# Kernel optimization log

Measured on AMD Instinct MI355X. Metric: run time of the kernel, lower is better.

The kernel has to match this reference:

```python
import jax, jax.numpy as jnp
import numpy as np

D_MODEL = 1024
N_HEADS = 16
HEAD_DIM = D_MODEL // N_HEADS
D_FF = 4096
ROPE_RANK = 16
LN_EPS = 1e-5


def _ln(x, g, b):
    mu = jnp.mean(x, axis=-1, keepdims=True)
    var = jnp.mean((x - mu) ** 2, axis=-1, keepdims=True)
    return (x - mu) * jax.lax.rsqrt(var + LN_EPS) * g + b


def _rope(x, A, B_):
    # x: [B, T, D]; learned low-rank additive correction to sin/cos tables
    B, T, D = x.shape
    pos = jnp.arange(T, dtype=jnp.float32)
    theta = 1.0 / (10000.0 ** (jnp.arange(0, D, 2, dtype=jnp.float32) / D))  # [D/2]
    angles = pos[:, None] * theta[None, :]                                   # [T, D/2]
    sin_pos, cos_pos = jnp.sin(angles), jnp.cos(angles)
    base = jnp.concatenate([sin_pos, cos_pos], axis=-1)                      # [T, D]
    learned = (base @ A) @ B_                                                # [T, D]
    l_sin, l_cos = jnp.split(learned, 2, axis=-1)
    sin_f = sin_pos + l_sin                                                  # [T, D/2]
    cos_f = cos_pos + l_cos
    xe, xo = x[..., ::2], x[..., 1::2]
    re = xe * cos_f[None] - xo * sin_f[None]
    ro = xe * sin_f[None] + xo * cos_f[None]
    return jnp.stack([re, ro], axis=-1).reshape(B, T, D)


def setup_inputs() -> dict:
    key = jax.random.key(0)
    ks = jax.random.split(key, 20)
    B, T = 2, 2048
    s = 1.0 / np.sqrt(D_MODEL)
    sf = 1.0 / np.sqrt(D_FF)
    sr = 1.0 / np.sqrt(ROPE_RANK)
    return {
        "tgt": jax.random.normal(ks[0], (B, T, D_MODEL), jnp.float32),
        "Wq": jax.random.normal(ks[1], (D_MODEL, D_MODEL), jnp.float32) * s,
        "bq": jnp.zeros((D_MODEL,), jnp.float32),
        "Wk": jax.random.normal(ks[2], (D_MODEL, D_MODEL), jnp.float32) * s,
        "bk": jnp.zeros((D_MODEL,), jnp.float32),
        "Wv": jax.random.normal(ks[3], (D_MODEL, D_MODEL), jnp.float32) * s,
        "bv": jnp.zeros((D_MODEL,), jnp.float32),
        "Wo": jax.random.normal(ks[4], (D_MODEL, D_MODEL), jnp.float32) * s,
        "bo": jnp.zeros((D_MODEL,), jnp.float32),
        "W1": jax.random.normal(ks[5], (D_MODEL, D_FF), jnp.float32) * s,
        "b1": jnp.zeros((D_FF,), jnp.float32),
        "W2": jax.random.normal(ks[6], (D_FF, D_MODEL), jnp.float32) * sf,
        "b2": jnp.zeros((D_MODEL,), jnp.float32),
        "ln1_g": jnp.ones((D_MODEL,), jnp.float32),
        "ln1_b": jnp.zeros((D_MODEL,), jnp.float32),
        "ln2_g": jnp.ones((D_MODEL,), jnp.float32),
        "ln2_b": jnp.zeros((D_MODEL,), jnp.float32),
        "rope_A": jax.random.normal(ks[7], (D_MODEL, ROPE_RANK), jnp.float32) * s,
        "rope_B": jax.random.normal(ks[8], (ROPE_RANK, D_MODEL), jnp.float32) * sr,
    }


def reference(tgt, Wq, bq, Wk, bk, Wv, bv, Wo, bo, W1, b1, W2, b2,
              ln1_g, ln1_b, ln2_g, ln2_b, rope_A, rope_B):
    x = tgt
    B, T, D = x.shape
    q = _rope(x @ Wq + bq, rope_A, rope_B)
    k = _rope(x @ Wk + bk, rope_A, rope_B)
    v = x @ Wv + bv
    # [B, H, T, hd]
    q = q.reshape(B, T, N_HEADS, HEAD_DIM).transpose(0, 2, 1, 3)
    k = k.reshape(B, T, N_HEADS, HEAD_DIM).transpose(0, 2, 1, 3)
    v = v.reshape(B, T, N_HEADS, HEAD_DIM).transpose(0, 2, 1, 3)
    scores = jnp.einsum("bhqd,bhkd->bhqk", q, k) / np.sqrt(HEAD_DIM)
    attn = jax.nn.softmax(scores, axis=-1)  # no mask: module applies none
    ctx = jnp.einsum("bhqk,bhkd->bhqd", attn, v)
    ctx = ctx.transpose(0, 2, 1, 3).reshape(B, T, D)
    x = x + (ctx @ Wo + bo)
    x = _ln(x, ln1_g, ln1_b)
    ff = jax.nn.relu(x @ W1 + b1) @ W2 + b2
    x = _ln(x + ff, ln2_g, ln2_b)
    return x
```

## Files before the change

### kernel.cpp

```cpp
#include <hip/hip_runtime.h>
#include <math.h>

typedef unsigned short u16;
typedef unsigned int u32;
typedef __attribute__((ext_vector_type(8))) short short8v;
typedef __attribute__((ext_vector_type(4))) float f32x4;

__device__ __forceinline__ u16 f2bf(float f) {
    u32 u = __float_as_uint(f);
    u32 r = (u + 0x7fffu + ((u >> 16) & 1u)) >> 16;
    return (u16)r;
}

#define GLOAD_LDS(g, l)                                                        \
    __builtin_amdgcn_global_load_lds(                                          \
        (const __attribute__((address_space(1))) void*)(g),                    \
        (__attribute__((address_space(3))) void*)(l), 16, 0, 0)

#define SCHED_FENCE() __builtin_amdgcn_sched_barrier(0)

#define ROPE_LOG2C (13.287712379549449f / 512.0f)

__device__ __forceinline__ void cast_body(const float* __restrict__ x,
                                          u16* __restrict__ y, int L, int tid) {
    const int gid = L * 256 + tid;
    float4 v = ((const float4*)x)[gid];
    ushort4 o;
    o.x = f2bf(v.x); o.y = f2bf(v.y); o.z = f2bf(v.z); o.w = f2bf(v.w);
    ((ushort4*)y)[gid] = o;
}

__device__ __forceinline__ void tcast64_body(const float* __restrict__ S,
                                             u16* __restrict__ Dt, int K, int N,
                                             int n0, int k0, int tid,
                                             char* smem) {
    float (*tile)[65] = (float (*)[65])smem;
    const int tx = tid & 15, ty = tid >> 4;
#pragma unroll
    for (int i = 0; i < 4; i++) {
        const int kr = ty + 16 * i;
        const float4 v = *(const float4*)&S[(size_t)(k0 + kr) * N + n0 + tx * 4];
        tile[kr][tx * 4 + 0] = v.x;
        tile[kr][tx * 4 + 1] = v.y;
        tile[kr][tx * 4 + 2] = v.z;
        tile[kr][tx * 4 + 3] = v.w;
    }
    __syncthreads();
#pragma unroll
    for (int i = 0; i < 4; i++) {
        const int nr = ty + 16 * i;
        ushort4 o;
        o.x = f2bf(tile[tx * 4 + 0][nr]);
        o.y = f2bf(tile[tx * 4 + 1][nr]);
        o.z = f2bf(tile[tx * 4 + 2][nr]);
        o.w = f2bf(tile[tx * 4 + 3][nr]);
        *(ushort4*)&Dt[(size_t)(n0 + nr) * K + k0 + tx * 4] = o;
    }
}

__device__ __forceinline__ void rope1_body(const float* __restrict__ A,
                                           float* __restrict__ P, int blk,
                                           int tid, char* smem) {
    float (*sc)[17]  = (float (*)[17])(smem);
    float (*cc)[17]  = (float (*)[17])(smem + 1088);
    float (*Als)[17] = (float (*)[17])(smem + 2176);
    float (*Alc)[17] = (float (*)[17])(smem + 3264);
    const int tt = tid >> 4, rr = tid & 15;
    const int t = blk * 16 + tt;
    float acc = 0.f;
    for (int i0 = 0; i0 < 512; i0 += 16) {
        __syncthreads();
        {
            const int i = i0 + rr;
            const float th = exp2f(-(float)i * ROPE_LOG2C);
            const float ang = (float)t * th;
            sc[tt][rr] = sinf(ang);
            cc[tt][rr] = cosf(ang);
            Als[tt][rr] = A[(i0 + tt) * 16 + rr];
            Alc[tt][rr] = A[(512 + i0 + tt) * 16 + rr];
        }
        __syncthreads();
#pragma unroll
        for (int ii = 0; ii < 16; ++ii)
            acc = fmaf(sc[tt][ii], Als[ii][rr],
                       fmaf(cc[tt][ii], Alc[ii][rr], acc));
    }
    P[t * 16 + rr] = acc;
}

__global__ __launch_bounds__(256) void prep_k(
    const float* __restrict__ tgt, u16* __restrict__ tgtb,
    const float* __restrict__ Wq, u16* __restrict__ Wqt,
    const float* __restrict__ Wk, u16* __restrict__ Wkt,
    const float* __restrict__ Wv, u16* __restrict__ Wvt,
    const float* __restrict__ Wo, u16* __restrict__ Wot,
    const float* __restrict__ W1, u16* __restrict__ W1t,
    const float* __restrict__ W2, u16* __restrict__ W2t,
    const float* __restrict__ rA, float* __restrict__ Pp) {
    __shared__ char smem[64 * 65 * 4];
    const int L = blockIdx.x, tid = threadIdx.x;
    if (L < 128) {
        rope1_body(rA, Pp, L, tid, smem);
    } else if (L < 4224) {
        cast_body(tgt, tgtb, L - 128, tid);
    } else if (L < 5248) {
        const int i = L - 4224;
        const int r = i >> 8, j = i & 255;
        const float* S = r == 0 ? Wq : (r == 1 ? Wk : (r == 2 ? Wv : Wo));
        u16* Dt = r == 0 ? Wqt : (r == 1 ? Wkt : (r == 2 ? Wvt : Wot));
        tcast64_body(S, Dt, 1024, 1024, (j & 15) * 64, (j >> 4) * 64, tid, smem);
    } else if (L < 6272) {
        const int j = L - 5248;
        tcast64_body(W1, W1t, 1024, 4096, (j & 63) * 64, (j >> 6) * 64, tid, smem);
    } else {
        const int j = L - 6272;
        tcast64_body(W2, W2t, 4096, 1024, (j & 15) * 64, (j >> 4) * 64, tid, smem);
    }
}

__global__ __launch_bounds__(256) void vtrans_k(const u16* __restrict__ vv,
                                                u16* __restrict__ Vt) {
    __shared__ u16 tile[32][33];
    const int key0 = blockIdx.x * 32, d0 = blockIdx.y * 32, bh = blockIdx.z;
    const int b = bh >> 4, h = bh & 15;
    const int tx = threadIdx.x & 31, ty = threadIdx.x >> 5;
#pragma unroll
    for (int i = 0; i < 4; i++)
        tile[ty + 8 * i][tx] =
            vv[(size_t)(b * 2048 + key0 + ty + 8 * i) * 1024 + h * 64 + d0 + tx];
    __syncthreads();
#pragma unroll
    for (int i = 0; i < 4; i++) {
        const int d = d0 + ty + 8 * i;
        const int key = key0 + tx;
        const int ksw = (key & ~63) | ((((key >> 3) & 7) ^ (d & 7)) << 3) | (key & 7);
        Vt[((size_t)bh * 64 + d) * 2048 + ksw] = tile[tx][ty + 8 * i];
    }
}

__global__ void rope2_k(const float* __restrict__ P, const float* __restrict__ Bw,
                        float* __restrict__ sf, float* __restrict__ cf) {
    const int gid = blockIdx.x * blockDim.x + threadIdx.x;
    if (gid >= 2048 * 512) return;
    const int t = gid >> 9, i = gid & 511;
    float ls = 0.f, lc = 0.f;
#pragma unroll
    for (int r = 0; r < 16; ++r) {
        const float p = P[t * 16 + r];
        ls = fmaf(p, Bw[r * 1024 + i], ls);
        lc = fmaf(p, Bw[r * 1024 + 512 + i], lc);
    }
    const float th = exp2f(-(float)i * ROPE_LOG2C);
    const float ang = (float)t * th;
    sf[gid] = sinf(ang) + ls;
    cf[gid] = cosf(ang) + lc;
}

__device__ __forceinline__ void xcd_tile(int L, int xn, int rn, int rm,
                                         int& tm, int& tn) {
    const int xcd = L & 7, i = L >> 3;
    const int cx = xcd % xn, cy = xcd / xn;
    tn = cx * rn + (i % rn);
    tm = cy * rm + (i / rn);
}

enum { EP_NONE = 0, EP_RELU = 3, EP_PART = 4 };

template <int EPI, bool CBF, int BN>
__global__ __launch_bounds__(256) void mgemm_k(
    const u16* __restrict__ A, const u16* __restrict__ Bt,
    const float* __restrict__ bias, void* __restrict__ Cp,
    void* __restrict__ Cp2, int M, int N, int K, int lda, int ldb,
    int xn, int rn, int rm, int mtiles) {
    constexpr int NT = BN / 32;
    __shared__ u16 As[3 * 128 * 32];
    __shared__ u16 Bs[3 * BN * 32];
    const int tid = threadIdx.x;
    const int w = tid >> 6, l = tid & 63;
    const int quad = l >> 4, lr = l & 15;
    const int wr = w >> 1, wc = w & 1;
    int tm, tn;
    xcd_tile(blockIdx.x, xn, rn, rm, tm, tn);
    int kh = 0;
    if (tm >= mtiles) { kh = 1; tm -= mtiles; }
    const u16* Ak = A + (size_t)kh * K;
    const u16* Bk = Bt + (size_t)kh * K;
    void* Co = kh ? Cp2 : Cp;
    const int m0 = tm * 128, n0 = tn * BN;

    const int srow = w * 16 + (l >> 2);
    const int scol = (((l & 3) ^ ((l >> 3) & 3)) * 8);
    const u16* ag0 = Ak + (size_t)(m0 + srow) * lda + scol;
    const u16* ag1 = Ak + (size_t)(m0 + 64 + srow) * lda + scol;
    const u16* bg0 = Bk + (size_t)(n0 + srow) * ldb + scol;
    const u16* bg1 = Bk + (size_t)(n0 + 64 + srow) * ldb + scol;

    f32x4 acc[4][NT];
#pragma unroll
    for (int i = 0; i < 4; i++)
#pragma unroll
        for (int j = 0; j < NT; j++) acc[i][j] = (f32x4)(0.0f);

    {
        GLOAD_LDS(ag0, As + w * 512);
        GLOAD_LDS(ag1, As + 2048 + w * 512);
        GLOAD_LDS(bg0, Bs + w * 512);
        if (BN == 128) GLOAD_LDS(bg1, Bs + 2048 + w * 512);
        GLOAD_LDS(ag0 + 32, As + 4096 + w * 512);
        GLOAD_LDS(ag1 + 32, As + 4096 + 2048 + w * 512);
        GLOAD_LDS(bg0 + 32, Bs + BN * 32 + w * 512);
        if (BN == 128) GLOAD_LDS(bg1 + 32, Bs + BN * 32 + 2048 + w * 512);
    }

    const int niter = K >> 5;
    const int xsw = ((lr >> 1) & 3) << 3;
    int bc = 0, bs = 2;
    for (int i = 0; i < niter; ++i) {
        SCHED_FENCE();
        if (i + 1 < niter) {
            if (BN == 128) asm volatile("s_waitcnt vmcnt(4) lgkmcnt(0)" ::: "memory");
            else           asm volatile("s_waitcnt vmcnt(3) lgkmcnt(0)" ::: "memory");
        } else {
            asm volatile("s_waitcnt vmcnt(0) lgkmcnt(0)" ::: "memory");
        }
        __builtin_amdgcn_s_barrier();
        SCHED_FENCE();
        if (i + 2 < niter) {
            const int kk = (i + 2) << 5;
            u16* Ab = As + bs * 4096;
            u16* Bb = Bs + bs * (BN * 32);
            GLOAD_LDS(ag0 + kk, Ab + w * 512);
            GLOAD_LDS(ag1 + kk, Ab + 2048 + w * 512);
            GLOAD_LDS(bg0 + kk, Bb + w * 512);
            if (BN == 128) GLOAD_LDS(bg1 + kk, Bb + 2048 + w * 512);
        }
        const u16* Ac = As + bc * 4096;
        const u16* Bc = Bs + bc * (BN * 32);
        short8v af[4], bf[NT];
#pragma unroll
        for (int mt = 0; mt < 4; ++mt)
            af[mt] = *(const short8v*)&Ac[(wr * 64 + mt * 16 + lr) * 32 +
                                          ((quad << 3) ^ xsw)];
#pragma unroll
        for (int nt = 0; nt < NT; ++nt)
            bf[nt] = *(const short8v*)&Bc[(wc * (BN / 2) + nt * 16 + lr) * 32 +
                                          ((quad << 3) ^ xsw)];
#pragma unroll
        for (int mt = 0; mt < 4; ++mt)
#pragma unroll
            for (int nt = 0; nt < NT; ++nt)
                acc[mt][nt] = __builtin_amdgcn_mfma_f32_16x16x32_bf16(
                    af[mt], bf[nt], acc[mt][nt], 0, 0, 0);
        bc = (bc == 2) ? 0 : bc + 1;
        bs = (bs == 2) ? 0 : bs + 1;
    }

#pragma unroll
    for (int mt = 0; mt < 4; ++mt) {
#pragma unroll
        for (int nt = 0; nt < NT; ++nt) {
            const int n = n0 + wc * (BN / 2) + nt * 16 + lr;
            const float bb = (EPI == EP_PART) ? 0.0f : bias[n];
#pragma unroll
            for (int reg = 0; reg < 4; ++reg) {
                const int m = m0 + wr * 64 + mt * 16 + quad * 4 + reg;
                float v = acc[mt][nt][reg] + bb;
                if (EPI == EP_RELU) v = fmaxf(v, 0.f);
                if (CBF) ((u16*)Co)[(size_t)m * N + n] = f2bf(v);
                else     ((float*)Co)[(size_t)m * N + n] = v;
            }
        }
    }
}

__global__ __launch_bounds__(256) void mqkv_k(
    const u16* __restrict__ A, const u16* __restrict__ Bt,
    const float* __restrict__ bq, const float* __restrict__ bk,
    const float* __restrict__ bv, const float* __restrict__ sf,
    const float* __restrict__ cf, u16* __restrict__ out) {
    const int K = 1024;
    __shared__ u16 As[3 * 128 * 32];
    __shared__ u16 Bs[3 * 128 * 32];
    const int tid = threadIdx.x;
    const int w = tid >> 6, l = tid & 63;
    const int quad = l >> 4, lr = l & 15;
    const int wr = w >> 1, wc = w & 1;
    int tm, tn;
    xcd_tile(blockIdx.x, 4, 6, 16, tm, tn);
    const int m0 = tm * 128, n0 = tn * 128;

    const int srow = w * 16 + (l >> 2);
    const int scol = (((l & 3) ^ ((l >> 3) & 3)) * 8);
    const u16* ag0 = A + (size_t)(m0 + srow) * K + scol;
    const u16* ag1 = A + (size_t)(m0 + 64 + srow) * K + scol;
    const u16* bg0 = Bt + (size_t)(n0 + srow) * K + scol;
    const u16* bg1 = Bt + (size_t)(n0 + 64 + srow) * K + scol;

    f32x4 acc[4][4];
#pragma unroll
    for (int i = 0; i < 4; i++)
#pragma unroll
        for (int j = 0; j < 4; j++) acc[i][j] = (f32x4)(0.0f);

    {
        GLOAD_LDS(ag0, As + w * 512);
        GLOAD_LDS(ag1, As + 2048 + w * 512);
        GLOAD_LDS(bg0, Bs + w * 512);
        GLOAD_LDS(bg1, Bs + 2048 + w * 512);
        GLOAD_LDS(ag0 + 32, As + 4096 + w * 512);
        GLOAD_LDS(ag1 + 32, As + 4096 + 2048 + w * 512);
        GLOAD_LDS(bg0 + 32, Bs + 4096 + w * 512);
        GLOAD_LDS(bg1 + 32, Bs + 4096 + 2048 + w * 512);
    }
    const int xsw = ((lr >> 1) & 3) << 3;
    int bc = 0, bsb = 2;
    for (int i = 0; i < 32; ++i) {
        SCHED_FENCE();
        if (i + 1 < 32) {
            asm volatile("s_waitcnt vmcnt(4) lgkmcnt(0)" ::: "memory");
        } else {
            asm volatile("s_waitcnt vmcnt(0) lgkmcnt(0)" ::: "memory");
        }
        __builtin_amdgcn_s_barrier();
        SCHED_FENCE();
        if (i + 2 < 32) {
            const int kk = (i + 2) << 5;
            u16* Ab = As + bsb * 4096;
            u16* Bb = Bs + bsb * 4096;
            GLOAD_LDS(ag0 + kk, Ab + w * 512);
            GLOAD_LDS(ag1 + kk, Ab + 2048 + w * 512);
            GLOAD_LDS(bg0 + kk, Bb + w * 512);
            GLOAD_LDS(bg1 + kk, Bb + 2048 + w * 512);
        }
        const u16* Ac = As + bc * 4096;
        const u16* Bc = Bs + bc * 4096;
        short8v af[4], bf[4];
#pragma unroll
        for (int mt = 0; mt < 4; ++mt)
            af[mt] = *(const short8v*)&Ac[(wr * 64 + mt * 16 + lr) * 32 +
                                          ((quad << 3) ^ xsw)];
#pragma unroll
        for (int nt = 0; nt < 4; ++nt)
            bf[nt] = *(const short8v*)&Bc[(wc * 64 + nt * 16 + lr) * 32 +
                                          ((quad << 3) ^ xsw)];
#pragma unroll
        for (int mt = 0; mt < 4; ++mt)
#pragma unroll
            for (int nt = 0; nt < 4; ++nt)
                acc[mt][nt] = __builtin_amdgcn_mfma_f32_16x16x32_bf16(
                    af[mt], bf[nt], acc[mt][nt], 0, 0, 0);
        bc = (bc == 2) ? 0 : bc + 1;
        bsb = (bsb == 2) ? 0 : bsb + 1;
    }

    const int which = n0 >> 10;
    const float* bias = which == 0 ? bq : (which == 1 ? bk : bv);
    const bool doRope = which < 2;
    u16* Cp = out + (size_t)which * 4096 * 1024;

#pragma unroll
    for (int mt = 0; mt < 4; ++mt) {
#pragma unroll
        for (int nt = 0; nt < 4; ++nt) {
            const int n = n0 + wc * 64 + nt * 16 + lr;
            const int col = n & 1023;
            const float bb = bias[col];
#pragma unroll
            for (int reg = 0; reg < 4; ++reg) {
                const int m = m0 + wr * 64 + mt * 16 + quad * 4 + reg;
                float v = acc[mt][nt][reg] + bb;
                const float partner = __shfl_xor(v, 1);
                int colw = col;
                if (doRope) {
                    const int t = m & 2047;
                    const int fi = col >> 1;
                    const float svv = sf[t * 512 + fi];
                    const float cvv = cf[t * 512 + fi];
                    v = (col & 1) ? fmaf(partner, svv, v * cvv)
                                  : fmaf(v, cvv, -partner * svv);
                    if (which == 0) v *= 0.125f;
                    colw = (col & ~63) | ((((col >> 3) & 7) ^ (m & 7)) << 3) |
                           (col & 7);
                }
                Cp[(size_t)m * 1024 + colw] = f2bf(v);
            }
        }
    }
}

__global__ __launch_bounds__(256, 3) void mattn_k(
    const u16* __restrict__ Q, const u16* __restrict__ Kg,
    const u16* __restrict__ Vt, u16* __restrict__ O) {
    __shared__ u16 QPs[128 * 64];
    __shared__ u16 Ks[2][64 * 64];
    __shared__ u16 Vs[2][64 * 64];
    const int tid = threadIdx.x;
    const int w = tid >> 6, l = tid & 63;
    const int quad = l >> 4, lr = l & 15;
    const int L = blockIdx.x;
    const int bh = (L & 7) * 4 + ((L >> 3) & 3);
    const int b = bh >> 4, h = bh & 15;
    const int row0 = (L >> 5) * 128;
    const size_t base = (size_t)b * 2048 * 1024 + (size_t)h * 64;
    const size_t vbase = (size_t)bh * 64 * 2048;

    const int dr = l >> 3;
    const int dc = (l & 7) * 8;
    const int g0 = w * 2, g1 = g0 + 1;
    const u16* kg0 = Kg + base + (size_t)(g0 * 8 + dr) * 1024 + dc;
    const u16* kg1 = Kg + base + (size_t)(g1 * 8 + dr) * 1024 + dc;
    const u16* vg0 = Vt + vbase + (size_t)(g0 * 8 + dr) * 2048 + dc;
    const u16* vg1 = Vt + vbase + (size_t)(g1 * 8 + dr) * 2048 + dc;

#pragma unroll
    for (int j = 0; j < 4; ++j) {
        const int g = w * 4 + j;
        GLOAD_LDS(Q + base + (size_t)(row0 + g * 8 + dr) * 1024 + dc,
                  QPs + g * 512);
    }
    GLOAD_LDS(kg0, Ks[0] + g0 * 512);
    GLOAD_LDS(kg1, Ks[0] + g1 * 512);
    GLOAD_LDS(vg0, Vs[0] + g0 * 512);
    GLOAD_LDS(vg1, Vs[0] + g1 * 512);
    __syncthreads();

    const int rsw = lr & 7;
    short8v qf[2][2];
#pragma unroll
    for (int ntq = 0; ntq < 2; ++ntq) {
        const int qr = w * 32 + ntq * 16 + lr;
#pragma unroll
        for (int kh = 0; kh < 2; ++kh)
            qf[ntq][kh] = *(const short8v*)&QPs[qr * 64 +
                (((kh * 4 + quad) ^ rsw) << 3)];
    }

    f32x4 o_acc[2][4];
#pragma unroll
    for (int i = 0; i < 2; ++i)
#pragma unroll
        for (int j = 0; j < 4; ++j) o_acc[i][j] = (f32x4)(0.0f);
    float lsum[2] = {0.f, 0.f};

    for (int i = 0; i < 32; ++i) {
        __syncthreads();
        if (i + 1 < 32) {
            const size_t kro = (size_t)((i + 1) << 6) * 1024;
            const int kco = (i + 1) << 6;
            u16* Kb = Ks[(i + 1) & 1];
            u16* Vb = Vs[(i + 1) & 1];
            GLOAD_LDS(kg0 + kro, Kb + g0 * 512);
            GLOAD_LDS(kg1 + kro, Kb + g1 * 512);
            GLOAD_LDS(vg0 + kco, Vb + g0 * 512);
            GLOAD_LDS(vg1 + kco, Vb + g1 * 512);
        }
        const u16* Kc = Ks[i & 1];
        const u16* Vc = Vs[i & 1];

        f32x4 s[4][2];
#pragma unroll
        for (int mt = 0; mt < 4; ++mt)
#pragma unroll
            for (int ntq = 0; ntq < 2; ++ntq) s[mt][ntq] = (f32x4)(0.0f);
#pragma unroll
        for (int mt = 0; mt < 4; ++mt) {
            const int kr = mt * 16 + lr;
            const short8v kf0 = *(const short8v*)&Kc[kr * 64 + ((quad ^ rsw) << 3)];
            const short8v kf1 = *(const short8v*)&Kc[kr * 64 + (((quad + 4) ^ rsw) << 3)];
#pragma unroll
            for (int ntq = 0; ntq < 2; ++ntq) {
                s[mt][ntq] = __builtin_amdgcn_mfma_f32_16x16x32_bf16(
                    kf0, qf[ntq][0], s[mt][ntq], 0, 0, 0);
                s[mt][ntq] = __builtin_amdgcn_mfma_f32_16x16x32_bf16(
                    kf1, qf[ntq][1], s[mt][ntq], 0, 0, 0);
            }
        }

#pragma unroll
        for (int ntq = 0; ntq < 2; ++ntq) {
            const int prow = w * 32 + ntq * 16 + lr;
#pragma unroll
            for (int mt = 0; mt < 4; ++mt) {
                const float e0 = __expf(s[mt][ntq][0]);
                const float e1 = __expf(s[mt][ntq][1]);
                const float e2 = __expf(s[mt][ntq][2]);
                const float e3 = __expf(s[mt][ntq][3]);
                lsum[ntq] += (e0 + e1) + (e2 + e3);
                u32 p01, p23;
                asm("v_cvt_pk_bf16_f32 %0, %1, %2" : "=v"(p01) : "v"(e0), "v"(e1));
                asm("v_cvt_pk_bf16_f32 %0, %1, %2" : "=v"(p23) : "v"(e2), "v"(e3));
                uint2 pv; pv.x = p01; pv.y = p23;
                *(uint2*)&QPs[prow * 64 +
                              (((mt * 2 + (quad >> 1)) ^ rsw) << 3) +
                              (quad & 1) * 4] = pv;
            }
        }

        short8v vf[4][2];
#pragma unroll
        for (int ntd = 0; ntd < 4; ++ntd) {
            const int vr = ntd * 16 + lr;
            vf[ntd][0] = *(const short8v*)&Vc[vr * 64 + ((quad ^ rsw) << 3)];
            vf[ntd][1] = *(const short8v*)&Vc[vr * 64 + (((quad + 4) ^ rsw) << 3)];
        }
        short8v pf[2][2];
#pragma unroll
        for (int mtq = 0; mtq < 2; ++mtq) {
            const int prow = w * 32 + mtq * 16 + lr;
            pf[mtq][0] = *(const short8v*)&QPs[prow * 64 + ((quad ^ rsw) << 3)];
            pf[mtq][1] = *(const short8v*)&QPs[prow * 64 + (((quad + 4) ^ rsw) << 3)];
        }
#pragma unroll
        for (int mtq = 0; mtq < 2; ++mtq)
#pragma unroll
            for (int ntd = 0; ntd < 4; ++ntd) {
                o_acc[mtq][ntd] = __builtin_amdgcn_mfma_f32_16x16x32_bf16(
                    pf[mtq][0], vf[ntd][0], o_acc[mtq][ntd], 0, 0, 0);
                o_acc[mtq][ntd] = __builtin_amdgcn_mfma_f32_16x16x32_bf16(
                    pf[mtq][1], vf[ntd][1], o_acc[mtq][ntd], 0, 0, 0);
            }
    }

    float rden[2];
#pragma unroll
    for (int ntq = 0; ntq < 2; ++ntq) {
        float t = lsum[ntq];
        t += __shfl_xor(t, 16);
        t += __shfl_xor(t, 32);
        rden[ntq] = 1.0f / t;
    }
#pragma unroll
    for (int mtq = 0; mtq < 2; ++mtq) {
#pragma unroll
        for (int reg = 0; reg < 4; ++reg) {
            const float dsc = __shfl(rden[mtq], quad * 4 + reg);
            const int m = row0 + w * 32 + mtq * 16 + quad * 4 + reg;
#pragma unroll
            for (int ntd = 0; ntd < 4; ++ntd)
                O[base + (size_t)m * 1024 + ntd * 16 + lr] =
                    f2bf(o_acc[mtq][ntd][reg] * dsc);
        }
    }
}

__global__ __launch_bounds__(256) void lnf_k(
    const float* __restrict__ X, const float* __restrict__ P0,
    const float* __restrict__ P1, const float* __restrict__ cb,
    const float* __restrict__ g, const float* __restrict__ bb,
    float* __restrict__ outf, u16* __restrict__ outb) {
    const int row = blockIdx.x, tid = threadIdx.x;
    const size_t off = (size_t)row * 1024 + tid * 4;
    float4 xv = *(const float4*)&X[off];
    float4 p0 = *(const float4*)&P0[off];
    float4 p1 = *(const float4*)&P1[off];
    float4 c4 = *(const float4*)&cb[tid * 4];
    xv.x += p0.x + p1.x + c4.x;
    xv.y += p0.y + p1.y + c4.y;
    xv.z += p0.z + p1.z + c4.z;
    xv.w += p0.w + p1.w + c4.w;
    float s = xv.x + xv.y + xv.z + xv.w;
    float s2 = xv.x * xv.x + xv.y * xv.y + xv.z * xv.z + xv.w * xv.w;
#pragma unroll
    for (int msk = 32; msk >= 1; msk >>= 1) {
        s += __shfl_xor(s, msk);
        s2 += __shfl_xor(s2, msk);
    }
    __shared__ float red[8];
    const int wv = tid >> 6;
    if ((tid & 63) == 0) { red[wv] = s; red[wv + 4] = s2; }
    __syncthreads();
    s = red[0] + red[1] + red[2] + red[3];
    s2 = red[4] + red[5] + red[6] + red[7];
    const float mu = s * (1.f / 1024.f);
    float var = s2 * (1.f / 1024.f) - mu * mu;
    var = fmaxf(var, 0.f);
    const float rstd = rsqrtf(var + 1e-5f);
    float4 g4 = *(const float4*)&g[tid * 4];
    float4 b4 = *(const float4*)&bb[tid * 4];
    float o0 = (xv.x - mu) * rstd * g4.x + b4.x;
    float o1 = (xv.y - mu) * rstd * g4.y + b4.y;
    float o2 = (xv.z - mu) * rstd * g4.z + b4.z;
    float o3 = (xv.w - mu) * rstd * g4.w + b4.w;
    if (outf)
        *(float4*)(outf + off) = make_float4(o0, o1, o2, o3);
    if (outb) {
        ushort4 ov;
        ov.x = f2bf(o0); ov.y = f2bf(o1); ov.z = f2bf(o2); ov.w = f2bf(o3);
        *(ushort4*)(outb + off) = ov;
    }
}

extern "C" void kernel_launch(void* const* d_in, const int* in_sizes, int n_in,
                              void* d_out, int out_size, void* d_ws, size_t ws_size,
                              hipStream_t stream) {
    const float* tgt = (const float*)d_in[0];
    const float* Wq  = (const float*)d_in[1];
    const float* bq  = (const float*)d_in[2];
    const float* Wk  = (const float*)d_in[3];
    const float* bk  = (const float*)d_in[4];
    const float* Wv  = (const float*)d_in[5];
    const float* bv  = (const float*)d_in[6];
    const float* Wo  = (const float*)d_in[7];
    const float* bo  = (const float*)d_in[8];
    const float* W1  = (const float*)d_in[9];
    const float* b1  = (const float*)d_in[10];
    const float* W2  = (const float*)d_in[11];
    const float* b2  = (const float*)d_in[12];
    const float* g1  = (const float*)d_in[13];
    const float* be1 = (const float*)d_in[14];
    const float* g2  = (const float*)d_in[15];
    const float* be2 = (const float*)d_in[16];
    const float* rA  = (const float*)d_in[17];
    const float* rB  = (const float*)d_in[18];

    const int M = 4096, D = 1024, DFF = 4096;
    const size_t MD = (size_t)M * D;
    const size_t MB = 1u << 20;
    char* wsb = (char*)d_ws;

    u16* q    = (u16*)wsb;
    u16* vv   = q + 2 * MD;
    u16* ctx  = (u16*)(wsb + 16 * MB);
    u16* Vt   = (u16*)(wsb + 24 * MB);
    u16* h    = q;
    float* PW0 = (float*)wsb;
    float* PW1 = (float*)(wsb + 32 * MB);
    float* PF0 = (float*)(wsb + 64 * MB);
    float* PF1 = (float*)(wsb + 32 * MB);
    float* sfp = (float*)(wsb + 32 * MB);
    float* cfp = sfp + (size_t)2048 * 512;
    u16* tgtb = (u16*)(wsb + 40 * MB);
    float* x1  = (float*)(wsb + 48 * MB);
    u16* x1b  = (u16*)(wsb + 64 * MB);
    u16* Wqt  = (u16*)(wsb + 64 * MB);
    u16* Wkt  = (u16*)(wsb + 66 * MB);
    u16* Wvt  = (u16*)(wsb + 68 * MB);
    u16* Wot  = (u16*)(wsb + 70 * MB);
    u16* W1t  = (u16*)(wsb + 72 * MB);
    u16* W2t  = (u16*)(wsb + 80 * MB);
    float* Pp = (float*)wsb;

    prep_k<<<dim3(7296), dim3(256), 0, stream>>>(
        tgt, tgtb, Wq, Wqt, Wk, Wkt, Wv, Wvt, Wo, Wot,
        W1, W1t, W2, W2t, rA, Pp);
    rope2_k<<<dim3(4096), dim3(256), 0, stream>>>(Pp, rB, sfp, cfp);

    mqkv_k<<<dim3(768), dim3(256), 0, stream>>>(
        tgtb, Wqt, bq, bk, bv, sfp, cfp, q);

    vtrans_k<<<dim3(64, 2, 32), dim3(256), 0, stream>>>(vv, Vt);

    mattn_k<<<dim3(512), dim3(256), 0, stream>>>(q, q + MD, Vt, ctx);

    mgemm_k<EP_PART, false, 128><<<dim3(512), dim3(256), 0, stream>>>(
        ctx, Wot, nullptr, PW0, PW1, M, D, 512, D, D, 1, 8, 8, 32);
    lnf_k<<<dim3(4096), dim3(256), 0, stream>>>(
        tgt, PW0, PW1, bo, g1, be1, x1, x1b);
    mgemm_k<EP_RELU, true, 128><<<dim3(1024), dim3(256), 0, stream>>>(
        x1b, W1t, b1, h, nullptr, M, DFF, D, D, D, 4, 8, 16, 1 << 20);
    mgemm_k<EP_PART, false, 128><<<dim3(512), dim3(256), 0, stream>>>(
        h, W2t, nullptr, PF0, PF1, M, D, 2048, DFF, DFF, 1, 8, 8, 32);
    lnf_k<<<dim3(4096), dim3(256), 0, stream>>>(
        x1, PF0, PF1, b2, g2, be2, (float*)d_out, nullptr);

    (void)in_sizes; (void)n_in; (void)out_size; (void)ws_size;
}
```

Before: 404.3 us.

## Use 256x256 eight-wave GEMM tiles for QKV and FFN1 projections

Result: slower. 420.0 us (+3.9%).

```diff
diff --git a/kernel.cpp b/kernel.cpp
--- a/kernel.cpp
+++ b/kernel.cpp
@@ -273,85 +273,135 @@
     }
 }
 
-__global__ __launch_bounds__(256) void mqkv_k(
+#define G8_DECL()                                                              \
+    const int tid = threadIdx.x;                                               \
+    const int w = tid >> 6, l = tid & 63;                                      \
+    const int quad = l >> 4, lr = l & 15;                                      \
+    const int wr = w >> 2, wc = w & 3;                                         \
+    const int lr7 = lr & 7;                                                    \
+    const int sg8 = (((l & 7) ^ ((l >> 3) & 7)) * 8);                          \
+    const int srow = w * 8 + (l >> 3);
+
+#define G8_HT(XS, GB, LD, KT, HH)                                              \
+    do {                                                                       \
+        GLOAD_LDS((GB) + (size_t)((HH) * 128 + srow) * (LD) + (KT) * 64 + sg8, \
+                  (XS) + ((HH) * 128 + w * 8) * 64);                           \
+        GLOAD_LDS((GB) + (size_t)((HH) * 128 + 64 + srow) * (LD) + (KT) * 64 + sg8,\
+                  (XS) + ((HH) * 128 + 64 + w * 8) * 64);                      \
+    } while (0)
+
+#define G8_DSB(BS)                                                             \
+    _Pragma("unroll") for (int nn = 0; nn < 4; ++nn)                           \
+        _Pragma("unroll") for (int kk = 0; kk < 2; ++kk)                       \
+            bfr[nn][kk] = *(const short8v*)&(BS)[(wc * 64 + nn * 16 + lr) * 64 \
+                + (((kk * 4 + quad) ^ lr7) << 3)];
+
+#define G8_DSA(AS, Q)                                                          \
+    _Pragma("unroll") for (int mm = 0; mm < 2; ++mm)                           \
+        _Pragma("unroll") for (int kk = 0; kk < 2; ++kk)                       \
+            af[mm][kk] = *(const short8v*)&(AS)[(wr * 128 + ((Q) * 2 + mm) * 16 + lr) * 64 \
+                + (((kk * 4 + quad) ^ lr7) << 3)];
+
+#define G8_MFMA(Q)                                                             \
+    __builtin_amdgcn_s_setprio(1);                                             \
+    _Pragma("unroll") for (int mm = 0; mm < 2; ++mm)                           \
+        _Pragma("unroll") for (int nn = 0; nn < 4; ++nn)                       \
+            _Pragma("unroll") for (int kk = 0; kk < 2; ++kk)                   \
+                acc[(Q) * 2 + mm][nn] = __builtin_amdgcn_mfma_f32_16x16x32_bf16(\
+                    af[mm][kk], bfr[nn][kk], acc[(Q) * 2 + mm][nn], 0, 0, 0);  \
+    __builtin_amdgcn_s_setprio(0);
+
+#define G8_PHASE(AS, BS, Q, RDB, STG, ENDW)                                    \
+    do {                                                                       \
+        SCHED_FENCE();                                                         \
+        if (RDB) { G8_DSB(BS); }                                               \
+        G8_DSA(AS, Q);                                                         \
+        STG;                                                                   \
+        SCHED_FENCE();                                                         \
+        if (RDB) asm volatile("s_waitcnt lgkmcnt(8)" ::: "memory");            \
+        __builtin_amdgcn_s_barrier();                                          \
+        asm volatile("s_waitcnt lgkmcnt(0)" ::: "memory");                     \
+        SCHED_FENCE();                                                         \
+        G8_MFMA(Q);                                                            \
+        SCHED_FENCE();                                                         \
+        ENDW;                                                                  \
+        __builtin_amdgcn_s_barrier();                                          \
+    } while (0)
+
+#define G8_VM4() asm volatile("s_waitcnt vmcnt(4)" ::: "memory")
+#define G8_VM0() asm volatile("s_waitcnt vmcnt(0)" ::: "memory")
+
+#define G8_LOOP(Ag, LDA, Bg, LDB)                                              \
+    f32x4 acc[8][4];                                                           \
+    _Pragma("unroll") for (int i = 0; i < 8; i++)                              \
+        _Pragma("unroll") for (int j = 0; j < 4; j++) acc[i][j] = (f32x4)(0.0f);\
+    short8v bfr[4][2], af[2][2];                                               \
+    u16* const As0 = &AsLds[0][0];                                             \
+    u16* const As1 = &AsLds[1][0];                                             \
+    u16* const Bs0 = &BsLds[0][0];                                             \
+    u16* const Bs1 = &BsLds[1][0];                                             \
+    G8_HT(Bs0, Bg, LDB, 0, 0); G8_HT(Bs0, Bg, LDB, 0, 1);                      \
+    G8_HT(As0, Ag, LDA, 0, 0); G8_HT(As0, Ag, LDA, 0, 1);                      \
+    G8_HT(Bs1, Bg, LDB, 1, 0); G8_HT(Bs1, Bg, LDB, 1, 1);                      \
+    G8_VM4();                                                                  \
+    __builtin_amdgcn_s_barrier();                                              \
+    for (int i = 0; i < 8; ++i) {                                              \
+        const int k1 = 2 * i + 1, k2 = 2 * i + 2, k3 = 2 * i + 3;              \
+        const bool full = (i < 7);                                             \
+        G8_PHASE(As0, Bs0, 0, true,  { G8_HT(As1, Ag, LDA, k1, 0); }, );       \
+        G8_PHASE(As0, Bs0, 1, false, { G8_HT(As1, Ag, LDA, k1, 1); }, );       \
+        G8_PHASE(As0, Bs0, 2, false, { if (full) G8_HT(Bs0, Bg, LDB, k2, 0); }, );\
+        G8_PHASE(As0, Bs0, 3, false, { if (full) G8_HT(Bs0, Bg, LDB, k2, 1); },\
+                 { if (full) G8_VM4(); else G8_VM0(); });                      \
+        G8_PHASE(As1, Bs1, 0, true,  { if (full) G8_HT(As0, Ag, LDA, k2, 0); }, );\
+        G8_PHASE(As1, Bs1, 1, false, { if (full) G8_HT(As0, Ag, LDA, k2, 1); }, );\
+        G8_PHASE(As1, Bs1, 2, false, { if (full) G8_HT(Bs1, Bg, LDB, k3, 0); }, );\
+        G8_PHASE(As1, Bs1, 3, false, { if (full) G8_HT(Bs1, Bg, LDB, k3, 1); },\
+                 { if (full) G8_VM4(); else G8_VM0(); });                      \
+    }
+
+__global__ __launch_bounds__(512, 2) void gffn1_k(
+    const u16* __restrict__ A, const u16* __restrict__ Bt,
+    const float* __restrict__ bias, u16* __restrict__ Cp) {
+    __shared__ u16 AsLds[2][256 * 64];
+    __shared__ u16 BsLds[2][256 * 64];
+    G8_DECL();
+    int tm, tn;
+    xcd_tile(blockIdx.x, 4, 4, 8, tm, tn);
+    const int m0 = tm * 256, n0 = tn * 256;
+    const u16* Ag = A + (size_t)m0 * 1024;
+    const u16* Bg = Bt + (size_t)n0 * 1024;
+    G8_LOOP(Ag, 1024, Bg, 1024);
+#pragma unroll
+    for (int mm = 0; mm < 8; ++mm) {
+#pragma unroll
+        for (int nn = 0; nn < 4; ++nn) {
+            const int n = n0 + wc * 64 + nn * 16 + lr;
+            const float bb = bias[n];
+#pragma unroll
+            for (int reg = 0; reg < 4; ++reg) {
+                const int m = m0 + wr * 128 + mm * 16 + quad * 4 + reg;
+                const float v = fmaxf(acc[mm][nn][reg] + bb, 0.f);
+                Cp[(size_t)m * 4096 + n] = f2bf(v);
+            }
+        }
+    }
+}
+
+__global__ __launch_bounds__(512, 2) void gqkv_k(
     const u16* __restrict__ A, const u16* __restrict__ Bt,
     const float* __restrict__ bq, const float* __restrict__ bk,
     const float* __restrict__ bv, const float* __restrict__ sf,
     const float* __restrict__ cf, u16* __restrict__ out) {
-    const int K = 1024;
-    __shared__ u16 As[3 * 128 * 32];
-    __shared__ u16 Bs[3 * 128 * 32];
-    const int tid = threadIdx.x;
-    const int w = tid >> 6, l = tid & 63;
-    const int quad = l >> 4, lr = l & 15;
-    const int wr = w >> 1, wc = w & 1;
+    __shared__ u16 AsLds[2][256 * 64];
+    __shared__ u16 BsLds[2][256 * 64];
+    G8_DECL();
     int tm, tn;
-    xcd_tile(blockIdx.x, 4, 6, 16, tm, tn);
-    const int m0 = tm * 128, n0 = tn * 128;
-
-    const int srow = w * 16 + (l >> 2);
-    const int scol = (((l & 3) ^ ((l >> 3) & 3)) * 8);
-    const u16* ag0 = A + (size_t)(m0 + srow) * K + scol;
-    const u16* ag1 = A + (size_t)(m0 + 64 + srow) * K + scol;
-    const u16* bg0 = Bt + (size_t)(n0 + srow) * K + scol;
-    const u16* bg1 = Bt + (size_t)(n0 + 64 + srow) * K + scol;
-
-    f32x4 acc[4][4];
-#pragma unroll
-    for (int i = 0; i < 4; i++)
-#pragma unroll
-        for (int j = 0; j < 4; j++) acc[i][j] = (f32x4)(0.0f);
-
-    {
-        GLOAD_LDS(ag0, As + w * 512);
-        GLOAD_LDS(ag1, As + 2048 + w * 512);
-        GLOAD_LDS(bg0, Bs + w * 512);
-        GLOAD_LDS(bg1, Bs + 2048 + w * 512);
-        GLOAD_LDS(ag0 + 32, As + 4096 + w * 512);
-        GLOAD_LDS(ag1 + 32, As + 4096 + 2048 + w * 512);
-        GLOAD_LDS(bg0 + 32, Bs + 4096 + w * 512);
-        GLOAD_LDS(bg1 + 32, Bs + 4096 + 2048 + w * 512);
-    }
-    const int xsw = ((lr >> 1) & 3) << 3;
-    int bc = 0, bsb = 2;
-    for (int i = 0; i < 32; ++i) {
-        SCHED_FENCE();
-        if (i + 1 < 32) {
-            asm volatile("s_waitcnt vmcnt(4) lgkmcnt(0)" ::: "memory");
-        } else {
-            asm volatile("s_waitcnt vmcnt(0) lgkmcnt(0)" ::: "memory");
-        }
-        __builtin_amdgcn_s_barrier();
-        SCHED_FENCE();
-        if (i + 2 < 32) {
-            const int kk = (i + 2) << 5;
-            u16* Ab = As + bsb * 4096;
-            u16* Bb = Bs + bsb * 4096;
-            GLOAD_LDS(ag0 + kk, Ab + w * 512);
-            GLOAD_LDS(ag1 + kk, Ab + 2048 + w * 512);
-            GLOAD_LDS(bg0 + kk, Bb + w * 512);
-            GLOAD_LDS(bg1 + kk, Bb + 2048 + w * 512);
-        }
-        const u16* Ac = As + bc * 4096;
-        const u16* Bc = Bs + bc * 4096;
-        short8v af[4], bf[4];
-#pragma unroll
-        for (int mt = 0; mt < 4; ++mt)
-            af[mt] = *(const short8v*)&Ac[(wr * 64 + mt * 16 + lr) * 32 +
-                                          ((quad << 3) ^ xsw)];
-#pragma unroll
-        for (int nt = 0; nt < 4; ++nt)
-            bf[nt] = *(const short8v*)&Bc[(wc * 64 + nt * 16 + lr) * 32 +
-                                          ((quad << 3) ^ xsw)];
-#pragma unroll
-        for (int mt = 0; mt < 4; ++mt)
-#pragma unroll
-            for (int nt = 0; nt < 4; ++nt)
-                acc[mt][nt] = __builtin_amdgcn_mfma_f32_16x16x32_bf16(
-                    af[mt], bf[nt], acc[mt][nt], 0, 0, 0);
-        bc = (bc == 2) ? 0 : bc + 1;
-        bsb = (bsb == 2) ? 0 : bsb + 1;
-    }
+    xcd_tile(blockIdx.x, 4, 3, 8, tm, tn);
+    const int m0 = tm * 256, n0 = tn * 256;
+    const u16* Ag = A + (size_t)m0 * 1024;
+    const u16* Bg = Bt + (size_t)n0 * 1024;
+    G8_LOOP(Ag, 1024, Bg, 1024);
 
     const int which = n0 >> 10;
     const float* bias = which == 0 ? bq : (which == 1 ? bk : bv);
@@ -359,16 +409,16 @@
     u16* Cp = out + (size_t)which * 4096 * 1024;
 
 #pragma unroll
-    for (int mt = 0; mt < 4; ++mt) {
-#pragma unroll
-        for (int nt = 0; nt < 4; ++nt) {
-            const int n = n0 + wc * 64 + nt * 16 + lr;
+    for (int mm = 0; mm < 8; ++mm) {
+#pragma unroll
+        for (int nn = 0; nn < 4; ++nn) {
+            const int n = n0 + wc * 64 + nn * 16 + lr;
             const int col = n & 1023;
             const float bb = bias[col];
 #pragma unroll
             for (int reg = 0; reg < 4; ++reg) {
-                const int m = m0 + wr * 64 + mt * 16 + quad * 4 + reg;
-                float v = acc[mt][nt][reg] + bb;
+                const int m = m0 + wr * 128 + mm * 16 + quad * 4 + reg;
+                float v = acc[mm][nn][reg] + bb;
                 const float partner = __shfl_xor(v, 1);
                 int colw = col;
                 if (doRope) {
@@ -645,7 +695,7 @@
         W1, W1t, W2, W2t, rA, Pp);
     rope2_k<<<dim3(4096), dim3(256), 0, stream>>>(Pp, rB, sfp, cfp);
 
-    mqkv_k<<<dim3(768), dim3(256), 0, stream>>>(
+    gqkv_k<<<dim3(192), dim3(512), 0, stream>>>(
         tgtb, Wqt, bq, bk, bv, sfp, cfp, q);
 
     vtrans_k<<<dim3(64, 2, 32), dim3(256), 0, stream>>>(vv, Vt);
@@ -656,8 +706,7 @@
         ctx, Wot, nullptr, PW0, PW1, M, D, 512, D, D, 1, 8, 8, 32);
     lnf_k<<<dim3(4096), dim3(256), 0, stream>>>(
         tgt, PW0, PW1, bo, g1, be1, x1, x1b);
-    mgemm_k<EP_RELU, true, 128><<<dim3(1024), dim3(256), 0, stream>>>(
-        x1b, W1t, b1, h, nullptr, M, DFF, D, D, D, 4, 8, 16, 1 << 20);
+    gffn1_k<<<dim3(256), dim3(512), 0, stream>>>(x1b, W1t, b1, h);
     mgemm_k<EP_PART, false, 128><<<dim3(512), dim3(256), 0, stream>>>(
         h, W2t, nullptr, PF0, PF1, M, D, 2048, DFF, DFF, 1, 8, 8, 32);
     lnf_k<<<dim3(4096), dim3(256), 0, stream>>>(
```
